# Kernel tuning notes

Measured on AMD Instinct MI355X. Metric: run time of the kernel, lower is better.

## Reference

```python
import jax, jax.numpy as jnp
import numpy as np

B, N, IN_F, OUT_F = 2, 4096, 256, 256
ALPHA = 0.2          # LeakyReLU negative slope
MASK_NEG = -9e15     # zero_vec fill for non-edges
SINK_NEG = -1e9      # small_tensor sink column


def setup_inputs() -> dict:
    key = jax.random.key(0)
    kx, kadj, kw, kbw, kai, kbi, kaj, kbj = jax.random.split(key, 8)
    x = jax.random.normal(kx, (B, N, IN_F), dtype=jnp.float32)
    adjs = (jax.random.uniform(kadj, (B, N, N)) < 0.01).astype(jnp.float32)
    # xavier_uniform with gain=1.414 for Linear weights (shape [out, in])
    def xavier(k, shape, gain=1.414):
        fan_out, fan_in = shape
        bound = gain * np.sqrt(6.0 / (fan_in + fan_out))
        return jax.random.uniform(k, shape, minval=-bound, maxval=bound, dtype=jnp.float32)
    W = xavier(kw, (OUT_F, IN_F))
    bW = jax.random.uniform(kbw, (OUT_F,), minval=-1/np.sqrt(IN_F), maxval=1/np.sqrt(IN_F), dtype=jnp.float32)
    wai = xavier(kai, (1, OUT_F))
    bai = jax.random.uniform(kbi, (1,), minval=-1/np.sqrt(OUT_F), maxval=1/np.sqrt(OUT_F), dtype=jnp.float32)
    waj = xavier(kaj, (1, OUT_F))
    baj = jax.random.uniform(kbj, (1,), minval=-1/np.sqrt(OUT_F), maxval=1/np.sqrt(OUT_F), dtype=jnp.float32)
    return {"x": x, "adjs": adjs, "W": W, "bW": bW,
            "wai": wai, "bai": bai, "waj": waj, "baj": baj}


def reference(x, adjs, W, bW, wai, bai, waj, baj):
    b, n, _ = adjs.shape
    z = jnp.einsum('bni,oi->bno', x, W) + bW                 # [B,N,OUT]
    ai = jnp.einsum('bno,ko->bnk', z, wai) + bai             # [B,N,1]
    aj = jnp.einsum('bno,ko->bnk', z, waj) + baj             # [B,N,1]
    # [ai,1] @ [1,aj]^T == ai_i + aj_j (broadcast add)
    e = ai + jnp.swapaxes(aj, 1, 2)                          # [B,N,N]
    e = jnp.where(e >= 0, e, ALPHA * e)                      # LeakyReLU
    att = jnp.where(adjs > 0, e, MASK_NEG)                   # adjacency mask
    # sink column trick: append -1e9 logit, softmax over N+1, drop sink
    sink = jnp.full((b, n, 1), SINK_NEG, dtype=att.dtype)
    att = jax.nn.softmax(jnp.concatenate([att, sink], axis=-1), axis=-1)[:, :, :n]
    # dropout p=0 in eval -> identity
    return jnp.einsum('bnm,bmo->bno', att, z)                # [B,N,OUT]
```

## Files before the change

kernel.cpp:

```cpp
#include <hip/hip_runtime.h>
#include <hip/hip_bf16.h>


#define NN   4096
#define OUTF 256
#define INF  256
#define CAP_E 128

typedef __attribute__((ext_vector_type(8))) short short8v;
typedef __attribute__((ext_vector_type(4))) float f32x4;

static __device__ __forceinline__ unsigned short f2bf(float f) {
    union { float f; unsigned u; } v; v.f = f;
    unsigned r = v.u + 0x7fffu + ((v.u >> 16) & 1u);
    return (unsigned short)(r >> 16);
}
static __device__ __forceinline__ float bf2f(unsigned short u) {
    union { unsigned u; float f; } v; v.u = ((unsigned)u) << 16; return v.f;
}

#define BM 64
#define BN 64
#define BK 64

__global__ __launch_bounds__(256) void gat_zgemm(
        const float* __restrict__ x, const float* __restrict__ W,
        const float* __restrict__ bW, const float* __restrict__ wai,
        const float* __restrict__ waj, unsigned short* __restrict__ zb,
        float* __restrict__ pai, float* __restrict__ paj) {
    __shared__ alignas(16) unsigned short As[BM * BK];
    __shared__ alignas(16) unsigned short Bs[BN * BK];
    const int tid  = threadIdx.x;
    const int lane = tid & 63;
    const int wid  = tid >> 6;
    const int rowBase = blockIdx.x * BM;
    const int colBase = blockIdx.y * BN;
    const int wm = (wid >> 1) * 32;
    const int wn = (wid & 1) * 32;
    const int sr = tid >> 4;
    const int sc = tid & 15;

    f32x4 acc[2][2] = {};

    for (int kk = 0; kk < INF; kk += BK) {
        #pragma unroll
        for (int pass = 0; pass < BM / 16; ++pass) {
            int r = pass * 16 + sr;
            const float4 v = *(const float4*)(&x[(size_t)(rowBase + r) * INF + kk + sc * 4]);
            int off = r * 128 + ((sc * 8) ^ ((r & 7) << 4));
            *(ushort4*)((char*)As + off) =
                make_ushort4(f2bf(v.x), f2bf(v.y), f2bf(v.z), f2bf(v.w));
        }
        #pragma unroll
        for (int pass = 0; pass < BN / 16; ++pass) {
            int r = pass * 16 + sr;
            const float4 v = *(const float4*)(&W[(size_t)(colBase + r) * INF + kk + sc * 4]);
            int off = r * 128 + ((sc * 8) ^ ((r & 7) << 4));
            *(ushort4*)((char*)Bs + off) =
                make_ushort4(f2bf(v.x), f2bf(v.y), f2bf(v.z), f2bf(v.w));
        }
        __syncthreads();
        #pragma unroll
        for (int ks = 0; ks < 2; ++ks) {
            short8v aF[2], bF[2];
            #pragma unroll
            for (int m = 0; m < 2; ++m) {
                int row = wm + m * 16 + (lane & 15);
                int cb  = (ks * 64 + ((lane >> 4) * 16)) ^ ((row & 7) << 4);
                aF[m] = *(const short8v*)((const char*)As + row * 128 + cb);
            }
            #pragma unroll
            for (int n = 0; n < 2; ++n) {
                int row = wn + n * 16 + (lane & 15);
                int cb  = (ks * 64 + ((lane >> 4) * 16)) ^ ((row & 7) << 4);
                bF[n] = *(const short8v*)((const char*)Bs + row * 128 + cb);
            }
            #pragma unroll
            for (int m = 0; m < 2; ++m)
                #pragma unroll
                for (int n = 0; n < 2; ++n)
                    acc[m][n] = __builtin_amdgcn_mfma_f32_16x16x32_bf16(
                        aF[m], bF[n], acc[m][n], 0, 0, 0);
        }
        __syncthreads();
    }
    const int r4 = (lane >> 4) * 4;
    const int cW = lane & 15;
    const int col0 = colBase + wn + cW;
    const int col1 = col0 + 16;
    const float b0 = bW[col0],  b1 = bW[col1];
    const float i0 = wai[col0], i1 = wai[col1];
    const float j0 = waj[col0], j1 = waj[col1];
    const int slot = blockIdx.y * 2 + (wid & 1);
    #pragma unroll
    for (int m = 0; m < 2; ++m) {
        #pragma unroll
        for (int r = 0; r < 4; ++r) {
            int row = rowBase + wm + m * 16 + r4 + r;
            float z0 = acc[m][0][r] + b0;
            float z1 = acc[m][1][r] + b1;
            zb[(size_t)row * OUTF + col0] = f2bf(z0);
            zb[(size_t)row * OUTF + col1] = f2bf(z1);
            float pi = z0 * i0 + z1 * i1;
            float pj = z0 * j0 + z1 * j1;
            #pragma unroll
            for (int s = 1; s < 16; s <<= 1) {
                pi += __shfl_xor(pi, s);
                pj += __shfl_xor(pj, s);
            }
            if (cW == 0) {
                pai[row * 8 + slot] = pi;
                paj[row * 8 + slot] = pj;
            }
        }
    }
}

__global__ __launch_bounds__(256) void gat_fused(
        const float* __restrict__ adj, const float* __restrict__ pai,
        const float* __restrict__ paj, const float* __restrict__ bai,
        const float* __restrict__ baj, const unsigned short* __restrict__ zb,
        float* __restrict__ out) {
    __shared__ unsigned short s_idx[4][CAP_E];
    __shared__ float          s_w[4][CAP_E];
    const int tid  = threadIdx.x;
    const int lane = tid & 63;
    const int wv   = tid >> 6;
    const int row  = blockIdx.x * 4 + wv;
    const int b    = row >> 12;

    const float4* arow = (const float4*)(adj + (size_t)row * NN);
    float4 vv[16];
    #pragma unroll
    for (int t = 0; t < 16; ++t) vv[t] = arow[t * 64 + lane];

    const float4* pa = (const float4*)(pai + row * 8);
    const float4 u = pa[0], v2 = pa[1];
    const float AI = (u.x + u.y + u.z + u.w) + (v2.x + v2.y + v2.z + v2.w)
                   + bai[0] + baj[0];

    unsigned short* si = s_idx[wv];
    int base = 0;
    #pragma unroll
    for (int t = 0; t < 16; ++t) {
        int pred = (vv[t].x > 0.f ? 1 : 0) | (vv[t].y > 0.f ? 2 : 0) |
                   (vv[t].z > 0.f ? 4 : 0) | (vv[t].w > 0.f ? 8 : 0);
        unsigned long long b0 = __ballot(pred & 1);
        unsigned long long b1 = __ballot((pred >> 1) & 1);
        unsigned long long b2 = __ballot((pred >> 2) & 1);
        unsigned long long b3 = __ballot((pred >> 3) & 1);
        unsigned long long below = (1ull << lane) - 1ull;
        int pos = base + __popcll(b0 & below) + __popcll(b1 & below) +
                         __popcll(b2 & below) + __popcll(b3 & below);
        int jb = (t * 64 + lane) * 4;
        if (pred & 1) { if (pos < CAP_E) si[pos] = (unsigned short)jb;       ++pos; }
        if (pred & 2) { if (pos < CAP_E) si[pos] = (unsigned short)(jb + 1); ++pos; }
        if (pred & 4) { if (pos < CAP_E) si[pos] = (unsigned short)(jb + 2); ++pos; }
        if (pred & 8) { if (pos < CAP_E) si[pos] = (unsigned short)(jb + 3); ++pos; }
        base += __popcll(b0) + __popcll(b1) + __popcll(b2) + __popcll(b3);
    }
    const int cnt = base > CAP_E ? CAP_E : base;
    __syncthreads();

    const bool h0 = lane < cnt, h1 = lane + 64 < cnt;
    int e0 = 0, e1 = 0;
    float a0 = -3e38f, a1 = -3e38f;
    const float* pjb = paj + ((size_t)(b << 12)) * 8;
    if (h0) {
        e0 = si[lane];
        const float4* q = (const float4*)(pjb + e0 * 8);
        float4 x0 = q[0], x1 = q[1];
        a0 = (x0.x + x0.y + x0.z + x0.w) + (x1.x + x1.y + x1.z + x1.w);
    }
    if (h1) {
        e1 = si[lane + 64];
        const float4* q = (const float4*)(pjb + e1 * 8);
        float4 x0 = q[0], x1 = q[1];
        a1 = (x0.x + x0.y + x0.z + x0.w) + (x1.x + x1.y + x1.z + x1.w);
    }
    float lm = fmaxf(a0, a1);
    #pragma unroll
    for (int s = 1; s < 64; s <<= 1) lm = fmaxf(lm, __shfl_xor(lm, s));
    const float tm = AI + lm;
    const float m = tm >= 0.f ? tm : 0.2f * tm;
    float w0 = 0.f, w1 = 0.f;
    if (h0) { float e = AI + a0; e = e >= 0.f ? e : 0.2f * e; w0 = __expf(e - m); }
    if (h1) { float e = AI + a1; e = e >= 0.f ? e : 0.2f * e; w1 = __expf(e - m); }
    float ls = w0 + w1;
    #pragma unroll
    for (int s = 1; s < 64; s <<= 1) ls += __shfl_xor(ls, s);
    const float inv = cnt ? 1.f / ls : 0.f;
    float* swv = s_w[wv];
    if (h0) swv[lane] = w0;
    if (h1) swv[lane + 64] = w1;
    __syncthreads();

    const unsigned short* zcol = zb + ((size_t)(b << 12)) * OUTF + lane * 4;
    float4 acc = make_float4(0.f, 0.f, 0.f, 0.f);
    int p = 0;
    for (; p + 4 <= cnt; p += 4) {
        int   g0 = si[p],  g1 = si[p + 1], g2 = si[p + 2], g3 = si[p + 3];
        float W0 = swv[p], W1 = swv[p + 1], W2 = swv[p + 2], W3 = swv[p + 3];
        ushort4 q0 = *(const ushort4*)(zcol + (size_t)g0 * OUTF);
        ushort4 q1 = *(const ushort4*)(zcol + (size_t)g1 * OUTF);
        ushort4 q2 = *(const ushort4*)(zcol + (size_t)g2 * OUTF);
        ushort4 q3 = *(const ushort4*)(zcol + (size_t)g3 * OUTF);
        acc.x = fmaf(W0, bf2f(q0.x), fmaf(W1, bf2f(q1.x), fmaf(W2, bf2f(q2.x), fmaf(W3, bf2f(q3.x), acc.x))));
        acc.y = fmaf(W0, bf2f(q0.y), fmaf(W1, bf2f(q1.y), fmaf(W2, bf2f(q2.y), fmaf(W3, bf2f(q3.y), acc.y))));
        acc.z = fmaf(W0, bf2f(q0.z), fmaf(W1, bf2f(q1.z), fmaf(W2, bf2f(q2.z), fmaf(W3, bf2f(q3.z), acc.z))));
        acc.w = fmaf(W0, bf2f(q0.w), fmaf(W1, bf2f(q1.w), fmaf(W2, bf2f(q2.w), fmaf(W3, bf2f(q3.w), acc.w))));
    }
    for (; p < cnt; ++p) {
        int g = si[p]; float Wp = swv[p];
        ushort4 q = *(const ushort4*)(zcol + (size_t)g * OUTF);
        acc.x = fmaf(Wp, bf2f(q.x), acc.x);
        acc.y = fmaf(Wp, bf2f(q.y), acc.y);
        acc.z = fmaf(Wp, bf2f(q.z), acc.z);
        acc.w = fmaf(Wp, bf2f(q.w), acc.w);
    }
    float4 r = make_float4(acc.x * inv, acc.y * inv, acc.z * inv, acc.w * inv);
    *(float4*)(out + (size_t)row * OUTF + lane * 4) = r;
}

extern "C" void kernel_launch(void* const* d_in, const int* in_sizes, int n_in,
                              void* d_out, int out_size, void* d_ws, size_t ws_size,
                              hipStream_t stream) {
    const float* x   = (const float*)d_in[0];
    const float* adj = (const float*)d_in[1];
    const float* W   = (const float*)d_in[2];
    const float* bW  = (const float*)d_in[3];
    const float* wai = (const float*)d_in[4];
    const float* bai = (const float*)d_in[5];
    const float* waj = (const float*)d_in[6];
    const float* baj = (const float*)d_in[7];
    float* out = (float*)d_out;

    char* ws = (char*)d_ws;
    unsigned short* zb = (unsigned short*)ws;
    float* pai = (float*)(ws + (4u << 20));
    float* paj = pai + 8192 * 8;

    gat_zgemm<<<dim3(8192 / BM, OUTF / BN), 256, 0, stream>>>(
        x, W, bW, wai, waj, zb, pai, paj);
    gat_fused<<<2048, 256, 0, stream>>>(adj, pai, paj, bai, baj, zb, out);
}
```

Before: 55.71 us.

## Process two rows per wave and prefetch second adjacency row during first attention

Each wave now handles one row from each batch, so half as many blocks are launched. The adjacency row for batch 1 is loaded into registers while the attention gather for the batch-0 row runs, which hides the streaming read latency of the large dense adjacency. The __syncthreads calls are dropped because each wave only uses its own shared-memory slice. launch_bounds is raised to 4 blocks per CU. Keeping 16 float4 registers live across the gather phase increases register pressure and may reduce occupancy or cause spills.

```diff
diff --git a/kernel.cpp b/kernel.cpp
--- a/kernel.cpp
+++ b/kernel.cpp
@@ -116,35 +116,14 @@
     }
 }
 
-__global__ __launch_bounds__(256) void gat_fused(
-        const float* __restrict__ adj, const float* __restrict__ pai,
-        const float* __restrict__ paj, const float* __restrict__ bai,
-        const float* __restrict__ baj, const unsigned short* __restrict__ zb,
-        float* __restrict__ out) {
-    __shared__ unsigned short s_idx[4][CAP_E];
-    __shared__ float          s_w[4][CAP_E];
-    const int tid  = threadIdx.x;
-    const int lane = tid & 63;
-    const int wv   = tid >> 6;
-    const int row  = blockIdx.x * 4 + wv;
-    const int b    = row >> 12;
-
-    const float4* arow = (const float4*)(adj + (size_t)row * NN);
-    float4 vv[16];
-    #pragma unroll
-    for (int t = 0; t < 16; ++t) vv[t] = arow[t * 64 + lane];
-
-    const float4* pa = (const float4*)(pai + row * 8);
-    const float4 u = pa[0], v2 = pa[1];
-    const float AI = (u.x + u.y + u.z + u.w) + (v2.x + v2.y + v2.z + v2.w)
-                   + bai[0] + baj[0];
-
-    unsigned short* si = s_idx[wv];
+static __device__ __forceinline__ int compact16(const float4 (&vv)[16], int lane,
+                                                unsigned short* __restrict__ si) {
     int base = 0;
     #pragma unroll
     for (int t = 0; t < 16; ++t) {
-        int pred = (vv[t].x > 0.f ? 1 : 0) | (vv[t].y > 0.f ? 2 : 0) |
-                   (vv[t].z > 0.f ? 4 : 0) | (vv[t].w > 0.f ? 8 : 0);
+        const float4 v = vv[t];
+        int pred = (v.x > 0.f ? 1 : 0) | (v.y > 0.f ? 2 : 0) |
+                   (v.z > 0.f ? 4 : 0) | (v.w > 0.f ? 8 : 0);
         unsigned long long b0 = __ballot(pred & 1);
         unsigned long long b1 = __ballot((pred >> 1) & 1);
         unsigned long long b2 = __ballot((pred >> 2) & 1);
@@ -159,22 +138,29 @@
         if (pred & 8) { if (pos < CAP_E) si[pos] = (unsigned short)(jb + 3); ++pos; }
         base += __popcll(b0) + __popcll(b1) + __popcll(b2) + __popcll(b3);
     }
-    const int cnt = base > CAP_E ? CAP_E : base;
-    __syncthreads();
+    return base > CAP_E ? CAP_E : base;
+}
+
+static __device__ __forceinline__ void attendRow(
+        int row, int b, int cnt, int lane,
+        unsigned short* __restrict__ si, float* __restrict__ swv,
+        const float* __restrict__ pai, const float* __restrict__ paj,
+        float bsum, const unsigned short* __restrict__ zb,
+        float* __restrict__ out) {
+    const float4* pa = (const float4*)(pai + row * 8);
+    const float4 u = pa[0], v2 = pa[1];
+    const float AI = (u.x + u.y + u.z + u.w) + (v2.x + v2.y + v2.z + v2.w) + bsum;
 
     const bool h0 = lane < cnt, h1 = lane + 64 < cnt;
-    int e0 = 0, e1 = 0;
     float a0 = -3e38f, a1 = -3e38f;
     const float* pjb = paj + ((size_t)(b << 12)) * 8;
     if (h0) {
-        e0 = si[lane];
-        const float4* q = (const float4*)(pjb + e0 * 8);
+        const float4* q = (const float4*)(pjb + si[lane] * 8);
         float4 x0 = q[0], x1 = q[1];
         a0 = (x0.x + x0.y + x0.z + x0.w) + (x1.x + x1.y + x1.z + x1.w);
     }
     if (h1) {
-        e1 = si[lane + 64];
-        const float4* q = (const float4*)(pjb + e1 * 8);
+        const float4* q = (const float4*)(pjb + si[lane + 64] * 8);
         float4 x0 = q[0], x1 = q[1];
         a1 = (x0.x + x0.y + x0.z + x0.w) + (x1.x + x1.y + x1.z + x1.w);
     }
@@ -190,10 +176,8 @@
     #pragma unroll
     for (int s = 1; s < 64; s <<= 1) ls += __shfl_xor(ls, s);
     const float inv = cnt ? 1.f / ls : 0.f;
-    float* swv = s_w[wv];
     if (h0) swv[lane] = w0;
     if (h1) swv[lane + 64] = w1;
-    __syncthreads();
 
     const unsigned short* zcol = zb + ((size_t)(b << 12)) * OUTF + lane * 4;
     float4 acc = make_float4(0.f, 0.f, 0.f, 0.f);
@@ -218,8 +202,41 @@
         acc.z = fmaf(Wp, bf2f(q.z), acc.z);
         acc.w = fmaf(Wp, bf2f(q.w), acc.w);
     }
-    float4 r = make_float4(acc.x * inv, acc.y * inv, acc.z * inv, acc.w * inv);
-    *(float4*)(out + (size_t)row * OUTF + lane * 4) = r;
+    *(float4*)(out + (size_t)row * OUTF + lane * 4) =
+        make_float4(acc.x * inv, acc.y * inv, acc.z * inv, acc.w * inv);
+}
+
+__global__ __launch_bounds__(256, 4) void gat_fused(
+        const float* __restrict__ adj, const float* __restrict__ pai,
+        const float* __restrict__ paj, const float* __restrict__ bai,
+        const float* __restrict__ baj, const unsigned short* __restrict__ zb,
+        float* __restrict__ out) {
+    __shared__ unsigned short s_idx[4][CAP_E];
+    __shared__ float          s_w[4][CAP_E];
+    const int tid  = threadIdx.x;
+    const int lane = tid & 63;
+    const int wv   = tid >> 6;
+    const int gw   = blockIdx.x * 4 + wv;
+    unsigned short* si = s_idx[wv];
+    float* swv = s_w[wv];
+
+    const float bsum = bai[0] + baj[0];
+
+    const float4* arowA = (const float4*)(adj + (size_t)gw * NN);
+    float4 vv[16];
+    #pragma unroll
+    for (int t = 0; t < 16; ++t) vv[t] = arowA[t * 64 + lane];
+
+    const int cntA = compact16(vv, lane, si);
+
+    const float4* arowB = (const float4*)(adj + ((size_t)gw + 4096) * NN);
+    #pragma unroll
+    for (int t = 0; t < 16; ++t) vv[t] = arowB[t * 64 + lane];
+
+    attendRow(gw, 0, cntA, lane, si, swv, pai, paj, bsum, zb, out);
+
+    const int cntB = compact16(vv, lane, si);
+    attendRow(gw + 4096, 1, cntB, lane, si, swv, pai, paj, bsum, zb, out);
 }
 
 extern "C" void kernel_launch(void* const* d_in, const int* in_sizes, int n_in,
@@ -242,5 +259,5 @@
 
     gat_zgemm<<<dim3(8192 / BM, OUTF / BN), 256, 0, stream>>>(
         x, W, bW, wai, waj, zb, pai, paj);
-    gat_fused<<<2048, 256, 0, stream>>>(adj, pai, paj, bai, baj, zb, out);
-}
+    gat_fused<<<1024, 256, 0, stream>>>(adj, pai, paj, bai, baj, zb, out);
+}
```

New measurement: 60.64 us. 8.9% more time.

## Move adjacency bitmask packing into GEMM kernel; attend reads compact bitmask

Applied to the files above, without the earlier changes.

The GEMM kernel now also streams the dense fp32 adjacency and packs it into a bitmask. Its 512 blocks each cover 64K elements, so the adjacency read overlaps the GEMM work instead of running after it. The attention kernel then reads one 64-bit word per lane and builds its edge list with a prefix scan and ctz loop, dropping the 16-wide ballot compaction and the block barriers. This adds a bitmask write and read through the workspace, and the GEMM blocks now carry the full adjacency-read bandwidth.

```diff
diff --git a/kernel.cpp b/kernel.cpp
--- a/kernel.cpp
+++ b/kernel.cpp
@@ -27,7 +27,8 @@
         const float* __restrict__ x, const float* __restrict__ W,
         const float* __restrict__ bW, const float* __restrict__ wai,
         const float* __restrict__ waj, unsigned short* __restrict__ zb,
-        float* __restrict__ pai, float* __restrict__ paj) {
+        float* __restrict__ pai, float* __restrict__ paj,
+        const float* __restrict__ adj, unsigned short* __restrict__ mask16) {
     __shared__ alignas(16) unsigned short As[BM * BK];
     __shared__ alignas(16) unsigned short Bs[BN * BK];
     const int tid  = threadIdx.x;
@@ -84,43 +85,64 @@
         }
         __syncthreads();
     }
-    const int r4 = (lane >> 4) * 4;
-    const int cW = lane & 15;
-    const int col0 = colBase + wn + cW;
-    const int col1 = col0 + 16;
-    const float b0 = bW[col0],  b1 = bW[col1];
-    const float i0 = wai[col0], i1 = wai[col1];
-    const float j0 = waj[col0], j1 = waj[col1];
-    const int slot = blockIdx.y * 2 + (wid & 1);
-    #pragma unroll
-    for (int m = 0; m < 2; ++m) {
-        #pragma unroll
-        for (int r = 0; r < 4; ++r) {
-            int row = rowBase + wm + m * 16 + r4 + r;
-            float z0 = acc[m][0][r] + b0;
-            float z1 = acc[m][1][r] + b1;
-            zb[(size_t)row * OUTF + col0] = f2bf(z0);
-            zb[(size_t)row * OUTF + col1] = f2bf(z1);
-            float pi = z0 * i0 + z1 * i1;
-            float pj = z0 * j0 + z1 * j1;
-            #pragma unroll
-            for (int s = 1; s < 16; s <<= 1) {
-                pi += __shfl_xor(pi, s);
-                pj += __shfl_xor(pj, s);
-            }
-            if (cW == 0) {
-                pai[row * 8 + slot] = pi;
-                paj[row * 8 + slot] = pj;
-            }
-        }
-    }
-}
-
-__global__ __launch_bounds__(256) void gat_fused(
-        const float* __restrict__ adj, const float* __restrict__ pai,
-        const float* __restrict__ paj, const float* __restrict__ bai,
-        const float* __restrict__ baj, const unsigned short* __restrict__ zb,
-        float* __restrict__ out) {
+    {
+        const int r4 = (lane >> 4) * 4;
+        const int cW = lane & 15;
+        const int col0 = colBase + wn + cW;
+        const int col1 = col0 + 16;
+        const float b0 = bW[col0],  b1 = bW[col1];
+        const float i0 = wai[col0], i1 = wai[col1];
+        const float j0 = waj[col0], j1 = waj[col1];
+        const int slot = blockIdx.y * 2 + (wid & 1);
+        #pragma unroll
+        for (int m = 0; m < 2; ++m) {
+            #pragma unroll
+            for (int r = 0; r < 4; ++r) {
+                int row = rowBase + wm + m * 16 + r4 + r;
+                float z0 = acc[m][0][r] + b0;
+                float z1 = acc[m][1][r] + b1;
+                zb[(size_t)row * OUTF + col0] = f2bf(z0);
+                zb[(size_t)row * OUTF + col1] = f2bf(z1);
+                float pi = z0 * i0 + z1 * i1;
+                float pj = z0 * j0 + z1 * j1;
+                #pragma unroll
+                for (int s = 1; s < 16; s <<= 1) {
+                    pi += __shfl_xor(pi, s);
+                    pj += __shfl_xor(pj, s);
+                }
+                if (cW == 0) {
+                    pai[row * 8 + slot] = pi;
+                    paj[row * 8 + slot] = pj;
+                }
+            }
+        }
+    }
+
+    {
+        const int bid = blockIdx.y * gridDim.x + blockIdx.x;
+        const size_t fbase = (size_t)bid * 65536;
+        #pragma unroll 2
+        for (int it = 0; it < 16; ++it) {
+            size_t F = fbase + (size_t)it * 4096 + wid * 1024 + lane * 16;
+            unsigned bits = 0;
+            #pragma unroll
+            for (int q = 0; q < 4; ++q) {
+                const float4 v = *(const float4*)(adj + F + q * 4);
+                bits |= (v.x > 0.f ? 1u : 0u) << (q * 4);
+                bits |= (v.y > 0.f ? 2u : 0u) << (q * 4);
+                bits |= (v.z > 0.f ? 4u : 0u) << (q * 4);
+                bits |= (v.w > 0.f ? 8u : 0u) << (q * 4);
+            }
+            mask16[F >> 4] = (unsigned short)bits;
+        }
+    }
+}
+
+__global__ __launch_bounds__(256) void gat_attend(
+        const unsigned long long* __restrict__ mask64,
+        const float* __restrict__ pai, const float* __restrict__ paj,
+        const float* __restrict__ bai, const float* __restrict__ baj,
+        const unsigned short* __restrict__ zb, float* __restrict__ out) {
     __shared__ unsigned short s_idx[4][CAP_E];
     __shared__ float          s_w[4][CAP_E];
     const int tid  = threadIdx.x;
@@ -128,53 +150,42 @@
     const int wv   = tid >> 6;
     const int row  = blockIdx.x * 4 + wv;
     const int b    = row >> 12;
-
-    const float4* arow = (const float4*)(adj + (size_t)row * NN);
-    float4 vv[16];
+    unsigned short* si = s_idx[wv];
+    float* swv = s_w[wv];
+
+    unsigned long long mm = mask64[(size_t)row * 64 + lane];
+    const int c = __popcll(mm);
+    int incl = c;
     #pragma unroll
-    for (int t = 0; t < 16; ++t) vv[t] = arow[t * 64 + lane];
+    for (int s = 1; s < 64; s <<= 1) {
+        int t = __shfl_up(incl, s);
+        if (lane >= s) incl += t;
+    }
+    const int cnt0 = __shfl(incl, 63);
+    const int cnt = cnt0 > CAP_E ? CAP_E : cnt0;
+    int pos = incl - c;
+    while (mm) {
+        int bit = __builtin_ctzll(mm);
+        if (pos < CAP_E) si[pos] = (unsigned short)(lane * 64 + bit);
+        ++pos;
+        mm &= mm - 1;
+    }
 
     const float4* pa = (const float4*)(pai + row * 8);
     const float4 u = pa[0], v2 = pa[1];
     const float AI = (u.x + u.y + u.z + u.w) + (v2.x + v2.y + v2.z + v2.w)
                    + bai[0] + baj[0];
 
-    unsigned short* si = s_idx[wv];
-    int base = 0;
-    #pragma unroll
-    for (int t = 0; t < 16; ++t) {
-        int pred = (vv[t].x > 0.f ? 1 : 0) | (vv[t].y > 0.f ? 2 : 0) |
-                   (vv[t].z > 0.f ? 4 : 0) | (vv[t].w > 0.f ? 8 : 0);
-        unsigned long long b0 = __ballot(pred & 1);
-        unsigned long long b1 = __ballot((pred >> 1) & 1);
-        unsigned long long b2 = __ballot((pred >> 2) & 1);
-        unsigned long long b3 = __ballot((pred >> 3) & 1);
-        unsigned long long below = (1ull << lane) - 1ull;
-        int pos = base + __popcll(b0 & below) + __popcll(b1 & below) +
-                         __popcll(b2 & below) + __popcll(b3 & below);
-        int jb = (t * 64 + lane) * 4;
-        if (pred & 1) { if (pos < CAP_E) si[pos] = (unsigned short)jb;       ++pos; }
-        if (pred & 2) { if (pos < CAP_E) si[pos] = (unsigned short)(jb + 1); ++pos; }
-        if (pred & 4) { if (pos < CAP_E) si[pos] = (unsigned short)(jb + 2); ++pos; }
-        if (pred & 8) { if (pos < CAP_E) si[pos] = (unsigned short)(jb + 3); ++pos; }
-        base += __popcll(b0) + __popcll(b1) + __popcll(b2) + __popcll(b3);
-    }
-    const int cnt = base > CAP_E ? CAP_E : base;
-    __syncthreads();
-
     const bool h0 = lane < cnt, h1 = lane + 64 < cnt;
-    int e0 = 0, e1 = 0;
     float a0 = -3e38f, a1 = -3e38f;
     const float* pjb = paj + ((size_t)(b << 12)) * 8;
     if (h0) {
-        e0 = si[lane];
-        const float4* q = (const float4*)(pjb + e0 * 8);
+        const float4* q = (const float4*)(pjb + si[lane] * 8);
         float4 x0 = q[0], x1 = q[1];
         a0 = (x0.x + x0.y + x0.z + x0.w) + (x1.x + x1.y + x1.z + x1.w);
     }
     if (h1) {
-        e1 = si[lane + 64];
-        const float4* q = (const float4*)(pjb + e1 * 8);
+        const float4* q = (const float4*)(pjb + si[lane + 64] * 8);
         float4 x0 = q[0], x1 = q[1];
         a1 = (x0.x + x0.y + x0.z + x0.w) + (x1.x + x1.y + x1.z + x1.w);
     }
@@ -190,10 +201,8 @@
     #pragma unroll
     for (int s = 1; s < 64; s <<= 1) ls += __shfl_xor(ls, s);
     const float inv = cnt ? 1.f / ls : 0.f;
-    float* swv = s_w[wv];
     if (h0) swv[lane] = w0;
     if (h1) swv[lane + 64] = w1;
-    __syncthreads();
 
     const unsigned short* zcol = zb + ((size_t)(b << 12)) * OUTF + lane * 4;
     float4 acc = make_float4(0.f, 0.f, 0.f, 0.f);
@@ -218,8 +227,8 @@
         acc.z = fmaf(Wp, bf2f(q.z), acc.z);
         acc.w = fmaf(Wp, bf2f(q.w), acc.w);
     }
-    float4 r = make_float4(acc.x * inv, acc.y * inv, acc.z * inv, acc.w * inv);
-    *(float4*)(out + (size_t)row * OUTF + lane * 4) = r;
+    *(float4*)(out + (size_t)row * OUTF + lane * 4) =
+        make_float4(acc.x * inv, acc.y * inv, acc.z * inv, acc.w * inv);
 }
 
 extern "C" void kernel_launch(void* const* d_in, const int* in_sizes, int n_in,
@@ -236,11 +245,13 @@
     float* out = (float*)d_out;
 
     char* ws = (char*)d_ws;
-    unsigned short* zb = (unsigned short*)ws;
+    unsigned short* zb   = (unsigned short*)ws;
     float* pai = (float*)(ws + (4u << 20));
     float* paj = pai + 8192 * 8;
+    unsigned short* mask = (unsigned short*)(ws + (5u << 20));
 
     gat_zgemm<<<dim3(8192 / BM, OUTF / BN), 256, 0, stream>>>(
-        x, W, bW, wai, waj, zb, pai, paj);
-    gat_fused<<<2048, 256, 0, stream>>>(adj, pai, paj, bai, baj, zb, out);
-}
+        x, W, bW, wai, waj, zb, pai, paj, adj, mask);
+    gat_attend<<<2048, 256, 0, stream>>>(
+        (const unsigned long long*)mask, pai, paj, bai, baj, zb, out);
+}
```

Measured after the change: 54.58 us. 1.02x faster.
